# Kernel tuning notes

Measured on AMD Instinct MI355X. Metric: run time of the kernel, lower is better.

Reference implementation:

```python
import jax, jax.numpy as jnp
import numpy as np

N = 50000      # nodes
E = 800000     # edges per view (before self loops)
F_IN = 256     # node feature dim
H = 4          # attention heads
C = 128        # hidden dim (per-head out_channels; concat=False -> mean over heads)
V = 3          # views
NEG_SLOPE = 0.2


def gat_view(x, edge_index, W, a_src, a_dst, b):
    """PyG-style GATConv(heads=H, concat=False) + ELU. Adds self loops."""
    n = x.shape[0]
    loops = jnp.arange(n, dtype=edge_index.dtype)
    src = jnp.concatenate([edge_index[0], loops])  # [E+N]
    dst = jnp.concatenate([edge_index[1], loops])
    h = (x @ W).reshape(n, H, C)                    # [N,H,C]
    s_src = jnp.sum(h * a_src, axis=-1)             # [N,H]
    s_dst = jnp.sum(h * a_dst, axis=-1)             # [N,H]
    e = jax.nn.leaky_relu(s_src[src] + s_dst[dst], NEG_SLOPE)  # [E+N,H]
    # segment softmax over incoming edges of each destination node
    m = jax.ops.segment_max(e, dst, num_segments=n)
    m = jnp.where(jnp.isfinite(m), m, 0.0)
    ex = jnp.exp(e - m[dst])
    denom = jax.ops.segment_sum(ex, dst, num_segments=n)
    alpha = ex / jnp.maximum(denom[dst], 1e-16)     # [E+N,H]
    out = jax.ops.segment_sum(h[src] * alpha[:, :, None], dst, num_segments=n)  # [N,H,C]
    return jax.nn.elu(out.mean(axis=1) + b)         # [N,C]


def setup_inputs() -> dict:
    key = jax.random.key(0)
    ks = jax.random.split(key, 12)
    d = {
        "x": jax.random.normal(ks[0], (N, F_IN), dtype=jnp.float32),
        "edge_index0": jax.random.randint(ks[1], (2, E), 0, N, dtype=jnp.int32),
        "edge_index1": jax.random.randint(ks[2], (2, E), 0, N, dtype=jnp.int32),
        "edge_index2": jax.random.randint(ks[3], (2, E), 0, N, dtype=jnp.int32),
        "W": jax.random.normal(ks[4], (V, F_IN, H * C), dtype=jnp.float32) * 0.05,
        "a_src": jax.random.normal(ks[5], (V, H, C), dtype=jnp.float32) * 0.05,
        "a_dst": jax.random.normal(ks[6], (V, H, C), dtype=jnp.float32) * 0.05,
        "b": jnp.zeros((V, C), dtype=jnp.float32),
        "fus_w": jax.random.normal(ks[7], (C, 1), dtype=jnp.float32) * 0.05,
        "fus_b": jnp.zeros((1,), dtype=jnp.float32),
        "cls_w1": jax.random.normal(ks[8], (C, C // 2), dtype=jnp.float32) * 0.05,
        "cls_b1": jnp.zeros((C // 2,), dtype=jnp.float32),
        "cls_w2": jax.random.normal(ks[9], (C // 2, 2), dtype=jnp.float32) * 0.05,
        "cls_b2": jnp.zeros((2,), dtype=jnp.float32),
    }
    return d


def reference(x, edge_index0, edge_index1, edge_index2, W, a_src, a_dst, b,
              fus_w, fus_b, cls_w1, cls_b1, cls_w2, cls_b2):
    eis = [edge_index0, edge_index1, edge_index2]
    views = [gat_view(x, eis[v], W[v], a_src[v], a_dst[v], b[v]) for v in range(V)]
    stacked = jnp.stack(views, axis=1)                     # [N,V,C]
    scores = jnp.squeeze(stacked @ fus_w, -1) + fus_b      # [N,V]
    weights = jax.nn.softmax(scores, axis=1)               # view attention
    fused = jnp.sum(stacked * weights[..., None], axis=1)  # [N,C]
    hcls = jax.nn.relu(fused @ cls_w1 + cls_b1)            # dropout = identity (eval)
    logits = hcls @ cls_w2 + cls_b2                        # [N,2]
    return logits, weights
```

## Files before the change

kernel.cpp:

```cpp
#include <hip/hip_runtime.h>
#include <math.h>

#define NN 50000
#define EE 800000
#define FIN 256
#define HH 4
#define CC 128
#define HC 512
#define VV 3

#define NB 196
#define SPB 256
#define CAP 4608
#define EPB 8192

typedef __attribute__((ext_vector_type(8))) short short8;
typedef __attribute__((ext_vector_type(4))) float f32x4;
typedef __attribute__((ext_vector_type(2))) float f32x2;

__device__ __forceinline__ float lrelu(float x){ return x > 0.f ? x : 0.2f*x; }

__device__ __forceinline__ unsigned short f2bf(float f){
  unsigned u = __float_as_uint(f);
  u += 0x7fffu + ((u >> 16) & 1);
  return (unsigned short)(u >> 16);
}
__device__ __forceinline__ float bf2f(short b){
  return __uint_as_float(((unsigned)b & 0xffffu) << 16);
}

__device__ __forceinline__ float wave_sum64(float v){
#pragma unroll
  for (int off = 32; off; off >>= 1) v += __shfl_xor(v, off);
  return v;
}

__device__ __forceinline__ void async16(void* lds, const void* g){
  __builtin_amdgcn_global_load_lds(
      (const __attribute__((address_space(1))) unsigned*)g,
      (__attribute__((address_space(3))) unsigned*)lds, 16, 0, 0);
}

__global__ __launch_bounds__(256) void cast_x(const float* __restrict__ x,
                                              unsigned short* __restrict__ xb){
  int t = blockIdx.x * 256 + threadIdx.x;
  float4 v = *(const float4*)&x[(size_t)t * 4];
  ushort4 o;
  o.x = f2bf(v.x); o.y = f2bf(v.y); o.z = f2bf(v.z); o.w = f2bf(v.w);
  *(ushort4*)&xb[(size_t)t * 4] = o;
}

__global__ __launch_bounds__(256) void prep_w_all(const float* __restrict__ W,
                                                  unsigned short* __restrict__ wp){
  int t = blockIdx.x * 256 + threadIdx.x;
  int v = t >> 17;
  int tl = t & 131071;
  int k = tl >> 9, n = tl & 511;
  wp[(size_t)v * (FIN * HC) + (size_t)(k >> 5) * (HC * 32) + n * 32 + (k & 31)] = f2bf(W[t]);
}

__global__ __launch_bounds__(256) void gemm_mfma_scores(
    const unsigned short* __restrict__ xb, const unsigned short* __restrict__ wp_all,
    unsigned char* __restrict__ hb_all,
    const float* __restrict__ a_src, const float* __restrict__ a_dst,
    float* __restrict__ ssrc_all, float* __restrict__ sdst_all){
  __shared__ short As[128 * 32];
  __shared__ short Bs[128 * 32];
  __shared__ float sred[2][128][2];
  int tid = threadIdx.x;
  int wave = tid >> 6, lane = tid & 63;
  int l16 = lane & 15, q = lane >> 4;
  int wr = wave >> 1, wc = wave & 1;
  int head = blockIdx.y, v = blockIdx.z;
  int rowBase = blockIdx.x * 128, colBase = head * 128;

  const unsigned short* wp = wp_all + (size_t)v * FIN * HC;
  unsigned char* hb = hb_all + (size_t)v * NN * HC;
  const float* a_src_v = a_src + v * HH * CC;
  const float* a_dst_v = a_dst + v * HH * CC;
  float* ssrc = ssrc_all + (size_t)v * NN * HH;
  float* sdst = sdst_all + (size_t)v * NN * HH;

  int off0 = wave * 2048 + lane * 16;
  int off1 = off0 + 1024;
  int arow0 = off0 >> 6, akb0 = (off0 & 63) >> 1;
  int arow1 = off1 >> 6, akb1 = (off1 & 63) >> 1;
  size_t ga0 = (size_t)min(rowBase + arow0, NN - 1) * FIN + akb0;
  size_t ga1 = (size_t)min(rowBase + arow1, NN - 1) * FIN + akb1;
  const unsigned short* wpc = wp + (size_t)colBase * 32;

  f32x4 acc[4][4] = {};
  for (int kt = 0; kt < 8; kt++){
    async16((char*)As + wave * 2048,        xb + ga0 + kt * 32);
    async16((char*)As + wave * 2048 + 1024, xb + ga1 + kt * 32);
    async16((char*)Bs + wave * 2048,        wpc + (size_t)kt * (HC * 32) + (off0 >> 1));
    async16((char*)Bs + wave * 2048 + 1024, wpc + (size_t)kt * (HC * 32) + (off1 >> 1));
    __syncthreads();
    short8 af[4], bf[4];
#pragma unroll
    for (int i = 0; i < 4; i++)
      af[i] = *(const short8*)&As[(wr * 64 + i * 16 + l16) * 32 + q * 8];
#pragma unroll
    for (int j = 0; j < 4; j++)
      bf[j] = *(const short8*)&Bs[(wc * 64 + j * 16 + l16) * 32 + q * 8];
#pragma unroll
    for (int i = 0; i < 4; i++)
#pragma unroll
      for (int j = 0; j < 4; j++)
        acc[i][j] = __builtin_amdgcn_mfma_f32_16x16x32_bf16(af[i], bf[j], acc[i][j], 0, 0, 0);
    __syncthreads();
  }
#pragma unroll
  for (int i = 0; i < 4; i++){
#pragma unroll
    for (int r = 0; r < 4; r++){
      int row = rowBase + wr * 64 + i * 16 + q * 4 + r;
      if (row < NN){
        int p01 = __builtin_amdgcn_cvt_pk_fp8_f32(acc[i][0][r], acc[i][1][r], 0, false);
        int p23 = __builtin_amdgcn_cvt_pk_fp8_f32(acc[i][2][r], acc[i][3][r], 0, false);
        size_t rb = (size_t)row * HC + colBase + wc * 64 + l16;
        hb[rb +  0] = (unsigned char)(p01 & 0xff);
        hb[rb + 16] = (unsigned char)((p01 >> 8) & 0xff);
        hb[rb + 32] = (unsigned char)(p23 & 0xff);
        hb[rb + 48] = (unsigned char)((p23 >> 8) & 0xff);
      }
    }
  }
  float asv[4], adv[4];
#pragma unroll
  for (int j = 0; j < 4; j++){
    int c = wc * 64 + j * 16 + l16;
    asv[j] = a_src_v[head * CC + c];
    adv[j] = a_dst_v[head * CC + c];
  }
  float ps[4][4], pd[4][4];
#pragma unroll
  for (int i = 0; i < 4; i++)
#pragma unroll
    for (int r = 0; r < 4; r++){
      float s = 0.f, d = 0.f;
#pragma unroll
      for (int j = 0; j < 4; j++){
        s = fmaf(acc[i][j][r], asv[j], s);
        d = fmaf(acc[i][j][r], adv[j], d);
      }
      ps[i][r] = s; pd[i][r] = d;
    }
#pragma unroll
  for (int off = 1; off < 16; off <<= 1)
#pragma unroll
    for (int i = 0; i < 4; i++)
#pragma unroll
      for (int r = 0; r < 4; r++){
        ps[i][r] += __shfl_xor(ps[i][r], off);
        pd[i][r] += __shfl_xor(pd[i][r], off);
      }
  if (l16 == 0){
#pragma unroll
    for (int i = 0; i < 4; i++)
#pragma unroll
      for (int r = 0; r < 4; r++){
        int rl = wr * 64 + i * 16 + q * 4 + r;
        sred[wc][rl][0] = ps[i][r];
        sred[wc][rl][1] = pd[i][r];
      }
  }
  __syncthreads();
  if (tid < 128){
    int row = rowBase + tid;
    if (row < NN){
      ssrc[row * HH + head] = sred[0][tid][0] + sred[1][tid][0];
      sdst[row * HH + head] = sred[0][tid][1] + sred[1][tid][1];
    }
  }
}

__global__ __launch_bounds__(256) void bucket_scatter(const int* __restrict__ e0,
    const int* __restrict__ e1, const int* __restrict__ e2,
    int* __restrict__ gcur, unsigned* __restrict__ pairs){
  int v = blockIdx.y;
  const int* ei = (v == 0) ? e0 : ((v == 1) ? e1 : e2);
  __shared__ int cnt[NB];
  __shared__ int base[NB];
  int tid = threadIdx.x;
  for (int i = tid; i < NB; i += 256) cnt[i] = 0;
  __syncthreads();
  int estart = blockIdx.x * EPB;
  int eend = min(estart + EPB, EE);
  for (int e = estart + tid; e < eend; e += 256)
    atomicAdd(&cnt[ei[EE + e] >> 8], 1);
  __syncthreads();
  for (int i = tid; i < NB; i += 256){
    int c = cnt[i];
    base[i] = (c > 0) ? atomicAdd(&gcur[v * NB + i], c) : 0;
    cnt[i] = 0;
  }
  __syncthreads();
  for (int e = estart + tid; e < eend; e += 256){
    int s = ei[e], d = ei[EE + e];
    int b = d >> 8;
    int off = base[b] + atomicAdd(&cnt[b], 1);
    if (off < CAP)
      pairs[(size_t)(v * NB + b) * CAP + off] = ((unsigned)(d & 255) << 16) | (unsigned)s;
  }
}

__global__ __launch_bounds__(256) void bucket_scan(const int* __restrict__ gcur,
                                                   int* __restrict__ bbase){
  int v = blockIdx.x;
  __shared__ int wsum[4];
  int tid = threadIdx.x, lane = tid & 63, wv = tid >> 6;
  int val = 0;
  if (tid < NB) val = min(gcur[v * NB + tid], CAP) + min(SPB, NN - tid * SPB);
  int x = val;
#pragma unroll
  for (int off = 1; off < 64; off <<= 1){
    int t = __shfl_up(x, off);
    if (lane >= off) x += t;
  }
  if (lane == 63) wsum[wv] = x;
  __syncthreads();
  int pre = 0;
#pragma unroll
  for (int w = 0; w < 4; w++) if (w < wv) pre += wsum[w];
  if (tid < NB) bbase[v * NB + tid] = pre + x - val;
}

__global__ __launch_bounds__(256) void bucket_csr(const int* __restrict__ gcur,
    const int* __restrict__ bbase, const unsigned* __restrict__ pairs,
    int* __restrict__ rowptr_all, int* __restrict__ colx_all){
  int v = blockIdx.y, b = blockIdx.x;
  int* rowptr = rowptr_all + v * (NN + 1);
  int* colx = colx_all + (size_t)v * (EE + NN);
  __shared__ int hist[SPB];
  __shared__ int wsum[4];
  __shared__ int lcol[CAP + SPB];
  int tid = threadIdx.x, lane = tid & 63, wv = tid >> 6;
  int node0 = b << 8;
  int nvalid = min(SPB, NN - node0);
  int cnt = min(gcur[v * NB + b], CAP);
  int base = bbase[v * NB + b];
  const unsigned* pp = pairs + (size_t)(v * NB + b) * CAP;
  hist[tid] = (tid < nvalid) ? 1 : 0;
  __syncthreads();
  for (int i = tid; i < cnt; i += 256)
    atomicAdd(&hist[pp[i] >> 16], 1);
  __syncthreads();
  int val = hist[tid];
  int x = val;
#pragma unroll
  for (int off = 1; off < 64; off <<= 1){
    int t = __shfl_up(x, off);
    if (lane >= off) x += t;
  }
  if (lane == 63) wsum[wv] = x;
  __syncthreads();
  int pre = 0;
#pragma unroll
  for (int w = 0; w < 4; w++) if (w < wv) pre += wsum[w];
  int excl = pre + x - val;
  __syncthreads();
  hist[tid] = excl + ((tid < nvalid) ? 1 : 0);
  if (tid < nvalid){
    rowptr[node0 + tid] = base + excl;
    lcol[excl] = node0 + tid;
  }
  __syncthreads();
  for (int i = tid; i < cnt; i += 256){
    unsigned p = pp[i];
    int pos = atomicAdd(&hist[p >> 16], 1);
    lcol[pos] = (int)(p & 0xffffu);
  }
  __syncthreads();
  int total = cnt + nvalid;
  for (int i = tid; i < total; i += 256) colx[base + i] = lcol[i];
  if (b == NB - 1 && tid == 0) rowptr[NN] = base + total;
}

__global__ __launch_bounds__(256) void aggregate(const unsigned char* __restrict__ hb_all,
    const float* __restrict__ ssrc_all, const float* __restrict__ sdst_all,
    const int* __restrict__ rowptr_all, const int* __restrict__ colx_all,
    const float* __restrict__ bb, unsigned short* __restrict__ vout_all){
  int v = blockIdx.y;
  const unsigned char* hb = hb_all + (size_t)v * NN * HC;
  const float* ssrc = ssrc_all + (size_t)v * NN * HH;
  const float* sdst = sdst_all + (size_t)v * NN * HH;
  const int* rowptr = rowptr_all + v * (NN + 1);
  const int* colx = colx_all + (size_t)v * (EE + NN);
  const float* bv = bb + v * CC;
  unsigned short* voutv = vout_all + (size_t)v * NN * CC;

  int wave = threadIdx.x >> 6, lane = threadIdx.x & 63;
  int node = blockIdx.x * 4 + wave;
  int start = rowptr[node];
  int deg = rowptr[node + 1] - start;
  int myh = lane >> 4;
  float sdh = sdst[node * HH + myh];
  float acc[8] = {0.f, 0.f, 0.f, 0.f, 0.f, 0.f, 0.f, 0.f};
  float dsum = 0.f;

#define AGG_FMA(CH, CE) { \
    f32x2 p0 = __builtin_amdgcn_cvt_pk_f32_fp8(CH.x, false); \
    f32x2 p1 = __builtin_amdgcn_cvt_pk_f32_fp8(CH.x, true); \
    f32x2 p2 = __builtin_amdgcn_cvt_pk_f32_fp8(CH.y, false); \
    f32x2 p3 = __builtin_amdgcn_cvt_pk_f32_fp8(CH.y, true); \
    acc[0] = fmaf(CE, p0[0], acc[0]); \
    acc[1] = fmaf(CE, p0[1], acc[1]); \
    acc[2] = fmaf(CE, p1[0], acc[2]); \
    acc[3] = fmaf(CE, p1[1], acc[3]); \
    acc[4] = fmaf(CE, p2[0], acc[4]); \
    acc[5] = fmaf(CE, p2[1], acc[5]); \
    acc[6] = fmaf(CE, p3[0], acc[6]); \
    acc[7] = fmaf(CE, p3[1], acc[7]); }

  if (deg <= 64){
    int cpre = (lane < deg) ? colx[start + lane] : 0;
    uint2 h0, h1, h2, h3, h4, h5, h6, h7;
    float s0, s1, s2, s3, s4, s5, s6, s7;
#define AGG_PRO(HP, SP, P) { \
    int sp = __shfl(cpre, min(P, deg - 1)); \
    HP = *(const uint2*)&hb[(size_t)(unsigned)(sp * HC) + lane * 8]; \
    SP = ssrc[sp * HH + myh]; }
    AGG_PRO(h0, s0, 0) AGG_PRO(h1, s1, 1) AGG_PRO(h2, s2, 2) AGG_PRO(h3, s3, 3)
    AGG_PRO(h4, s4, 4) AGG_PRO(h5, s5, 5) AGG_PRO(h6, s6, 6) AGG_PRO(h7, s7, 7)
#undef AGG_PRO
#define AGG_STEP(HP, SP, P) { \
    float ce = __expf(lrelu(SP + sdh)); \
    dsum += ce; \
    uint2 ch = HP; \
    int ni = i + 8 + P; \
    if (ni < deg){ \
      int ns = __shfl(cpre, ni); \
      HP = *(const uint2*)&hb[(size_t)(unsigned)(ns * HC) + lane * 8]; \
      SP = ssrc[ns * HH + myh]; \
    } \
    AGG_FMA(ch, ce) }
    int i = 0;
    for (; i + 8 <= deg; i += 8){
      AGG_STEP(h0, s0, 0) AGG_STEP(h1, s1, 1) AGG_STEP(h2, s2, 2) AGG_STEP(h3, s3, 3)
      AGG_STEP(h4, s4, 4) AGG_STEP(h5, s5, 5) AGG_STEP(h6, s6, 6) AGG_STEP(h7, s7, 7)
    }
#undef AGG_STEP
    int rem = deg - i;
#define AGG_TAIL(HP, SP, P) if (rem > P){ \
    float ce = __expf(lrelu(SP + sdh)); \
    dsum += ce; \
    AGG_FMA(HP, ce) }
    AGG_TAIL(h0, s0, 0) AGG_TAIL(h1, s1, 1) AGG_TAIL(h2, s2, 2) AGG_TAIL(h3, s3, 3)
    AGG_TAIL(h4, s4, 4) AGG_TAIL(h5, s5, 5) AGG_TAIL(h6, s6, 6)
#undef AGG_TAIL
  } else {
    for (int i = 0; i < deg; i++){
      int src = colx[start + i];
      float sv = ssrc[src * HH + myh];
      float ce = __expf(lrelu(sv + sdh));
      dsum += ce;
      uint2 ch = *(const uint2*)&hb[(size_t)(unsigned)(src * HC) + lane * 8];
      AGG_FMA(ch, ce)
    }
  }
#undef AGG_FMA
  float rinv = 0.25f / fmaxf(dsum, 1e-16f);
#pragma unroll
  for (int j = 0; j < 8; j++) acc[j] *= rinv;
#pragma unroll
  for (int off = 16; off < 64; off <<= 1){
#pragma unroll
    for (int j = 0; j < 8; j++) acc[j] += __shfl_xor(acc[j], off);
  }
  if (lane < 16){
    int c0 = lane * 8;
    short8 o;
#pragma unroll
    for (int j = 0; j < 8; j++){
      float vv = acc[j] + bv[c0 + j];
      float e = vv > 0.f ? vv : (__expf(vv) - 1.f);
      o[j] = (short)f2bf(e);
    }
    *(short8*)&voutv[(size_t)node * CC + c0] = o;
  }
}

__global__ __launch_bounds__(256) void fuse_classify(const unsigned short* __restrict__ vb,
    const float* __restrict__ fw, const float* __restrict__ fb,
    const float* __restrict__ w1, const float* __restrict__ b1,
    const float* __restrict__ w2, const float* __restrict__ b2,
    float* __restrict__ out){
  __shared__ float sw1[CC * 64];
  __shared__ float sfused[4][CC];
  int tid = threadIdx.x;
  for (int i = tid * 4; i < CC * 64; i += 1024)
    *(float4*)&sw1[i] = *(const float4*)&w1[i];
  __syncthreads();
  int wave = tid >> 6, lane = tid & 63;
  int node = blockIdx.x * 4 + wave;
  unsigned r0 = *(const unsigned*)&vb[(size_t)(0 * NN + node) * CC + lane * 2];
  unsigned r1 = *(const unsigned*)&vb[(size_t)(1 * NN + node) * CC + lane * 2];
  unsigned r2 = *(const unsigned*)&vb[(size_t)(2 * NN + node) * CC + lane * 2];
  float v0x = bf2f((short)(r0 & 0xffffu)), v0y = bf2f((short)(r0 >> 16));
  float v1x = bf2f((short)(r1 & 0xffffu)), v1y = bf2f((short)(r1 >> 16));
  float v2x = bf2f((short)(r2 & 0xffffu)), v2y = bf2f((short)(r2 >> 16));
  float fwa = fw[lane * 2], fwb = fw[lane * 2 + 1];
  float s0 = wave_sum64(v0x * fwa + v0y * fwb) + fb[0];
  float s1 = wave_sum64(v1x * fwa + v1y * fwb) + fb[0];
  float s2 = wave_sum64(v2x * fwa + v2y * fwb) + fb[0];
  float mx = fmaxf(s0, fmaxf(s1, s2));
  float e0 = __expf(s0 - mx), e1 = __expf(s1 - mx), e2 = __expf(s2 - mx);
  float rs = 1.f / (e0 + e1 + e2);
  float w0 = e0 * rs, w1v = e1 * rs, w2v = e2 * rs;
  float f0 = w0 * v0x + w1v * v1x + w2v * v2x;
  float f1 = w0 * v0y + w1v * v1y + w2v * v2y;
  sfused[wave][lane * 2]     = f0;
  sfused[wave][lane * 2 + 1] = f1;
  if (lane < 3){
    float wv = (lane == 0) ? w0 : ((lane == 1) ? w1v : w2v);
    out[2 * NN + node * 3 + lane] = wv;
  }
  __syncthreads();
  float hc = b1[lane];
#pragma unroll 8
  for (int c = 0; c < CC; c++)
    hc = fmaf(sfused[wave][c], sw1[c * 64 + lane], hc);
  hc = fmaxf(hc, 0.f);
  float l0 = wave_sum64(hc * w2[lane * 2]);
  float l1 = wave_sum64(hc * w2[lane * 2 + 1]);
  if (lane == 0){
    out[node * 2]     = l0 + b2[0];
    out[node * 2 + 1] = l1 + b2[1];
  }
}

extern "C" void kernel_launch(void* const* d_in, const int* in_sizes, int n_in,
                              void* d_out, int out_size, void* d_ws, size_t ws_size,
                              hipStream_t stream){
  const float* x      = (const float*)d_in[0];
  const int*   e0     = (const int*)d_in[1];
  const int*   e1     = (const int*)d_in[2];
  const int*   e2     = (const int*)d_in[3];
  const float* W      = (const float*)d_in[4];
  const float* a_src  = (const float*)d_in[5];
  const float* a_dst  = (const float*)d_in[6];
  const float* bb     = (const float*)d_in[7];
  const float* fus_w  = (const float*)d_in[8];
  const float* fus_b  = (const float*)d_in[9];
  const float* cls_w1 = (const float*)d_in[10];
  const float* cls_b1 = (const float*)d_in[11];
  const float* cls_w2 = (const float*)d_in[12];
  const float* cls_b2 = (const float*)d_in[13];
  float* out = (float*)d_out;

  unsigned short* xb = (unsigned short*)d_ws;
  unsigned char* hb  = (unsigned char*)(xb + (size_t)NN * FIN);
  unsigned short* wp = (unsigned short*)(hb + (size_t)VV * NN * HC);
  float* ssrc = (float*)(wp + (size_t)VV * FIN * HC);
  float* sdst = ssrc + (size_t)VV * NN * HH;
  int* gcur   = (int*)(sdst + (size_t)VV * NN * HH);
  int* bbase  = gcur + VV * NB;
  int* rowptr = bbase + VV * NB;
  int* colx   = rowptr + VV * (NN + 1);
  unsigned* pairs = (unsigned*)(colx + (size_t)VV * (EE + NN));
  unsigned short* voutb = (unsigned short*)pairs;

  hipMemsetAsync(gcur, 0, (size_t)VV * NB * sizeof(int), stream);
  cast_x<<<12500, 256, 0, stream>>>(x, xb);
  prep_w_all<<<1536, 256, 0, stream>>>(W, wp);
  dim3 p1grid((EE + EPB - 1) / EPB, 3);
  bucket_scatter<<<p1grid, 256, 0, stream>>>(e0, e1, e2, gcur, pairs);
  bucket_scan<<<3, 256, 0, stream>>>(gcur, bbase);
  dim3 p2grid(NB, 3);
  bucket_csr<<<p2grid, 256, 0, stream>>>(gcur, bbase, pairs, rowptr, colx);

  dim3 ggrid(391, 4, 3);
  gemm_mfma_scores<<<ggrid, 256, 0, stream>>>(xb, wp, hb, a_src, a_dst, ssrc, sdst);
  dim3 agrid(12500, 3);
  aggregate<<<agrid, 256, 0, stream>>>(hb, ssrc, sdst, rowptr, colx, bb, voutb);
  fuse_classify<<<12500, 256, 0, stream>>>(voutb, fus_w, fus_b, cls_w1, cls_b1,
                                           cls_w2, cls_b2, out);
}
```

Before: 545.4 us.

## Load GEMM fragments directly with register double-buffering, pre-scale CSR indices, batch fuse_classify nodes

The GEMM drops its LDS staging and barriers and instead loads MFMA fragments straight from global memory into registers, double-buffered across k-steps. CSR column indices are stored pre-multiplied by 4, so the aggregate kernel computes addresses with shifts, and its separate high-degree path is folded into one prefetching loop that reads colx once the degree exceeds 64. The aggregate FMAs use packed f32x2 operations. fuse_classify processes 8 node groups per block so the W1 copy into LDS is amortised, and the bucket scatter uses a smaller EPB. Risks: no A/B reuse through LDS means more global traffic in the GEMM, and the __syncthreads before reading sfused is replaced by a waitcnt, which relies on each wave reading only its own row.

```diff
diff --git a/kernel.cpp b/kernel.cpp
--- a/kernel.cpp
+++ b/kernel.cpp
@@ -12,13 +12,11 @@
 #define NB 196
 #define SPB 256
 #define CAP 4608
-#define EPB 8192
+#define EPB 2048
 
 typedef __attribute__((ext_vector_type(8))) short short8;
 typedef __attribute__((ext_vector_type(4))) float f32x4;
 typedef __attribute__((ext_vector_type(2))) float f32x2;
-
-__device__ __forceinline__ float lrelu(float x){ return x > 0.f ? x : 0.2f*x; }
 
 __device__ __forceinline__ unsigned short f2bf(float f){
   unsigned u = __float_as_uint(f);
@@ -33,12 +31,6 @@
 #pragma unroll
   for (int off = 32; off; off >>= 1) v += __shfl_xor(v, off);
   return v;
-}
-
-__device__ __forceinline__ void async16(void* lds, const void* g){
-  __builtin_amdgcn_global_load_lds(
-      (const __attribute__((address_space(1))) unsigned*)g,
-      (__attribute__((address_space(3))) unsigned*)lds, 16, 0, 0);
 }
 
 __global__ __launch_bounds__(256) void cast_x(const float* __restrict__ x,
@@ -64,8 +56,6 @@
     unsigned char* __restrict__ hb_all,
     const float* __restrict__ a_src, const float* __restrict__ a_dst,
     float* __restrict__ ssrc_all, float* __restrict__ sdst_all){
-  __shared__ short As[128 * 32];
-  __shared__ short Bs[128 * 32];
   __shared__ float sred[2][128][2];
   int tid = threadIdx.x;
   int wave = tid >> 6, lane = tid & 63;
@@ -81,34 +71,40 @@
   float* ssrc = ssrc_all + (size_t)v * NN * HH;
   float* sdst = sdst_all + (size_t)v * NN * HH;
 
-  int off0 = wave * 2048 + lane * 16;
-  int off1 = off0 + 1024;
-  int arow0 = off0 >> 6, akb0 = (off0 & 63) >> 1;
-  int arow1 = off1 >> 6, akb1 = (off1 & 63) >> 1;
-  size_t ga0 = (size_t)min(rowBase + arow0, NN - 1) * FIN + akb0;
-  size_t ga1 = (size_t)min(rowBase + arow1, NN - 1) * FIN + akb1;
-  const unsigned short* wpc = wp + (size_t)colBase * 32;
-
+  const unsigned short* ap[4];
+  const unsigned short* bp[4];
+#pragma unroll
+  for (int i = 0; i < 4; i++){
+    int row = min(rowBase + wr * 64 + i * 16 + l16, NN - 1);
+    ap[i] = xb + (size_t)row * FIN + q * 8;
+  }
+#pragma unroll
+  for (int j = 0; j < 4; j++){
+    int col = colBase + wc * 64 + j * 16 + l16;
+    bp[j] = wp + (size_t)col * 32 + q * 8;
+  }
+  short8 af[2][4], bf[2][4];
+#pragma unroll
+  for (int i = 0; i < 4; i++){
+    af[0][i] = *(const short8*)(ap[i]);
+    bf[0][i] = *(const short8*)(bp[i]);
+  }
   f32x4 acc[4][4] = {};
+#pragma unroll
   for (int kt = 0; kt < 8; kt++){
-    async16((char*)As + wave * 2048,        xb + ga0 + kt * 32);
-    async16((char*)As + wave * 2048 + 1024, xb + ga1 + kt * 32);
-    async16((char*)Bs + wave * 2048,        wpc + (size_t)kt * (HC * 32) + (off0 >> 1));
-    async16((char*)Bs + wave * 2048 + 1024, wpc + (size_t)kt * (HC * 32) + (off1 >> 1));
-    __syncthreads();
-    short8 af[4], bf[4];
+    int cur = kt & 1, nxt = cur ^ 1;
+    if (kt < 7){
+#pragma unroll
+      for (int i = 0; i < 4; i++){
+        af[nxt][i] = *(const short8*)(ap[i] + (kt + 1) * 32);
+        bf[nxt][i] = *(const short8*)(bp[i] + (size_t)(kt + 1) * (HC * 32));
+      }
+    }
 #pragma unroll
     for (int i = 0; i < 4; i++)
-      af[i] = *(const short8*)&As[(wr * 64 + i * 16 + l16) * 32 + q * 8];
-#pragma unroll
-    for (int j = 0; j < 4; j++)
-      bf[j] = *(const short8*)&Bs[(wc * 64 + j * 16 + l16) * 32 + q * 8];
-#pragma unroll
-    for (int i = 0; i < 4; i++)
 #pragma unroll
       for (int j = 0; j < 4; j++)
-        acc[i][j] = __builtin_amdgcn_mfma_f32_16x16x32_bf16(af[i], bf[j], acc[i][j], 0, 0, 0);
-    __syncthreads();
+        acc[i][j] = __builtin_amdgcn_mfma_f32_16x16x32_bf16(af[cur][i], bf[cur][j], acc[i][j], 0, 0, 0);
   }
 #pragma unroll
   for (int i = 0; i < 4; i++){
@@ -263,13 +259,13 @@
   hist[tid] = excl + ((tid < nvalid) ? 1 : 0);
   if (tid < nvalid){
     rowptr[node0 + tid] = base + excl;
-    lcol[excl] = node0 + tid;
+    lcol[excl] = (node0 + tid) << 2;
   }
   __syncthreads();
   for (int i = tid; i < cnt; i += 256){
     unsigned p = pp[i];
     int pos = atomicAdd(&hist[p >> 16], 1);
-    lcol[pos] = (int)(p & 0xffffu);
+    lcol[pos] = (int)(p & 0xffffu) << 2;
   }
   __syncthreads();
   int total = cnt + nvalid;
@@ -287,93 +283,82 @@
   const float* sdst = sdst_all + (size_t)v * NN * HH;
   const int* rowptr = rowptr_all + v * (NN + 1);
   const int* colx = colx_all + (size_t)v * (EE + NN);
-  const float* bv = bb + v * CC;
-  unsigned short* voutv = vout_all + (size_t)v * NN * CC;
 
   int wave = threadIdx.x >> 6, lane = threadIdx.x & 63;
   int node = blockIdx.x * 4 + wave;
   int start = rowptr[node];
   int deg = rowptr[node + 1] - start;
   int myh = lane >> 4;
+  int l8 = lane * 8;
   float sdh = sdst[node * HH + myh];
-  float acc[8] = {0.f, 0.f, 0.f, 0.f, 0.f, 0.f, 0.f, 0.f};
+  f32x2 acc2[4] = {};
   float dsum = 0.f;
-
-#define AGG_FMA(CH, CE) { \
-    f32x2 p0 = __builtin_amdgcn_cvt_pk_f32_fp8(CH.x, false); \
-    f32x2 p1 = __builtin_amdgcn_cvt_pk_f32_fp8(CH.x, true); \
-    f32x2 p2 = __builtin_amdgcn_cvt_pk_f32_fp8(CH.y, false); \
-    f32x2 p3 = __builtin_amdgcn_cvt_pk_f32_fp8(CH.y, true); \
-    acc[0] = fmaf(CE, p0[0], acc[0]); \
-    acc[1] = fmaf(CE, p0[1], acc[1]); \
-    acc[2] = fmaf(CE, p1[0], acc[2]); \
-    acc[3] = fmaf(CE, p1[1], acc[3]); \
-    acc[4] = fmaf(CE, p2[0], acc[4]); \
-    acc[5] = fmaf(CE, p2[1], acc[5]); \
-    acc[6] = fmaf(CE, p3[0], acc[6]); \
-    acc[7] = fmaf(CE, p3[1], acc[7]); }
-
-  if (deg <= 64){
-    int cpre = (lane < deg) ? colx[start + lane] : 0;
-    uint2 h0, h1, h2, h3, h4, h5, h6, h7;
-    float s0, s1, s2, s3, s4, s5, s6, s7;
+  int cpre = (lane < deg) ? colx[start + lane] : 0;
+  uint2 h0, h1, h2, h3, h4, h5, h6, h7;
+  float s0, s1, s2, s3, s4, s5, s6, s7;
 #define AGG_PRO(HP, SP, P) { \
-    int sp = __shfl(cpre, min(P, deg - 1)); \
-    HP = *(const uint2*)&hb[(size_t)(unsigned)(sp * HC) + lane * 8]; \
-    SP = ssrc[sp * HH + myh]; }
-    AGG_PRO(h0, s0, 0) AGG_PRO(h1, s1, 1) AGG_PRO(h2, s2, 2) AGG_PRO(h3, s3, 3)
-    AGG_PRO(h4, s4, 4) AGG_PRO(h5, s5, 5) AGG_PRO(h6, s6, 6) AGG_PRO(h7, s7, 7)
+    int sp4 = __shfl(cpre, min(P, deg - 1)); \
+    HP = *(const uint2*)&hb[((size_t)(unsigned)sp4 << 7) + l8]; \
+    SP = ssrc[sp4 + myh]; }
+  AGG_PRO(h0, s0, 0) AGG_PRO(h1, s1, 1) AGG_PRO(h2, s2, 2) AGG_PRO(h3, s3, 3)
+  AGG_PRO(h4, s4, 4) AGG_PRO(h5, s5, 5) AGG_PRO(h6, s6, 6) AGG_PRO(h7, s7, 7)
 #undef AGG_PRO
+#define AGG_FMA(CH, E2) { \
+    acc2[0] = __builtin_elementwise_fma(E2, __builtin_amdgcn_cvt_pk_f32_fp8(CH.x, false), acc2[0]); \
+    acc2[1] = __builtin_elementwise_fma(E2, __builtin_amdgcn_cvt_pk_f32_fp8(CH.x, true),  acc2[1]); \
+    acc2[2] = __builtin_elementwise_fma(E2, __builtin_amdgcn_cvt_pk_f32_fp8(CH.y, false), acc2[2]); \
+    acc2[3] = __builtin_elementwise_fma(E2, __builtin_amdgcn_cvt_pk_f32_fp8(CH.y, true),  acc2[3]); }
 #define AGG_STEP(HP, SP, P) { \
-    float ce = __expf(lrelu(SP + sdh)); \
+    float xx = SP + sdh; \
+    float ce = __expf(fmaxf(xx, 0.2f * xx)); \
     dsum += ce; \
     uint2 ch = HP; \
     int ni = i + 8 + P; \
     if (ni < deg){ \
-      int ns = __shfl(cpre, ni); \
-      HP = *(const uint2*)&hb[(size_t)(unsigned)(ns * HC) + lane * 8]; \
-      SP = ssrc[ns * HH + myh]; \
+      int sp4; \
+      if (ni < 64) sp4 = __shfl(cpre, ni); else sp4 = colx[start + ni]; \
+      HP = *(const uint2*)&hb[((size_t)(unsigned)sp4 << 7) + l8]; \
+      SP = ssrc[sp4 + myh]; \
     } \
-    AGG_FMA(ch, ce) }
-    int i = 0;
-    for (; i + 8 <= deg; i += 8){
-      AGG_STEP(h0, s0, 0) AGG_STEP(h1, s1, 1) AGG_STEP(h2, s2, 2) AGG_STEP(h3, s3, 3)
-      AGG_STEP(h4, s4, 4) AGG_STEP(h5, s5, 5) AGG_STEP(h6, s6, 6) AGG_STEP(h7, s7, 7)
-    }
+    f32x2 e2 = {ce, ce}; \
+    AGG_FMA(ch, e2) }
+#define AGG_TAIL(HP, SP, P) if (rem > P){ \
+    float xx = SP + sdh; \
+    float ce = __expf(fmaxf(xx, 0.2f * xx)); \
+    dsum += ce; \
+    f32x2 e2 = {ce, ce}; \
+    AGG_FMA(HP, e2) }
+  int i = 0;
+  for (; i + 8 <= deg; i += 8){
+    AGG_STEP(h0, s0, 0) AGG_STEP(h1, s1, 1) AGG_STEP(h2, s2, 2) AGG_STEP(h3, s3, 3)
+    AGG_STEP(h4, s4, 4) AGG_STEP(h5, s5, 5) AGG_STEP(h6, s6, 6) AGG_STEP(h7, s7, 7)
+  }
+  int rem = deg - i;
+  AGG_TAIL(h0, s0, 0) AGG_TAIL(h1, s1, 1) AGG_TAIL(h2, s2, 2) AGG_TAIL(h3, s3, 3)
+  AGG_TAIL(h4, s4, 4) AGG_TAIL(h5, s5, 5) AGG_TAIL(h6, s6, 6)
 #undef AGG_STEP
-    int rem = deg - i;
-#define AGG_TAIL(HP, SP, P) if (rem > P){ \
-    float ce = __expf(lrelu(SP + sdh)); \
-    dsum += ce; \
-    AGG_FMA(HP, ce) }
-    AGG_TAIL(h0, s0, 0) AGG_TAIL(h1, s1, 1) AGG_TAIL(h2, s2, 2) AGG_TAIL(h3, s3, 3)
-    AGG_TAIL(h4, s4, 4) AGG_TAIL(h5, s5, 5) AGG_TAIL(h6, s6, 6)
 #undef AGG_TAIL
-  } else {
-    for (int i = 0; i < deg; i++){
-      int src = colx[start + i];
-      float sv = ssrc[src * HH + myh];
-      float ce = __expf(lrelu(sv + sdh));
-      dsum += ce;
-      uint2 ch = *(const uint2*)&hb[(size_t)(unsigned)(src * HC) + lane * 8];
-      AGG_FMA(ch, ce)
-    }
-  }
 #undef AGG_FMA
   float rinv = 0.25f / fmaxf(dsum, 1e-16f);
-#pragma unroll
-  for (int j = 0; j < 8; j++) acc[j] *= rinv;
+  float accs[8];
+#pragma unroll
+  for (int j = 0; j < 4; j++){
+    accs[2 * j]     = acc2[j][0] * rinv;
+    accs[2 * j + 1] = acc2[j][1] * rinv;
+  }
 #pragma unroll
   for (int off = 16; off < 64; off <<= 1){
 #pragma unroll
-    for (int j = 0; j < 8; j++) acc[j] += __shfl_xor(acc[j], off);
+    for (int j = 0; j < 8; j++) accs[j] += __shfl_xor(accs[j], off);
   }
   if (lane < 16){
+    const float* bv = bb + v * CC;
+    unsigned short* voutv = vout_all + (size_t)v * NN * CC;
     int c0 = lane * 8;
     short8 o;
 #pragma unroll
     for (int j = 0; j < 8; j++){
-      float vv = acc[j] + bv[c0 + j];
+      float vv = accs[j] + bv[c0 + j];
       float e = vv > 0.f ? vv : (__expf(vv) - 1.f);
       o[j] = (short)f2bf(e);
     }
@@ -393,40 +378,46 @@
     *(float4*)&sw1[i] = *(const float4*)&w1[i];
   __syncthreads();
   int wave = tid >> 6, lane = tid & 63;
-  int node = blockIdx.x * 4 + wave;
-  unsigned r0 = *(const unsigned*)&vb[(size_t)(0 * NN + node) * CC + lane * 2];
-  unsigned r1 = *(const unsigned*)&vb[(size_t)(1 * NN + node) * CC + lane * 2];
-  unsigned r2 = *(const unsigned*)&vb[(size_t)(2 * NN + node) * CC + lane * 2];
-  float v0x = bf2f((short)(r0 & 0xffffu)), v0y = bf2f((short)(r0 >> 16));
-  float v1x = bf2f((short)(r1 & 0xffffu)), v1y = bf2f((short)(r1 >> 16));
-  float v2x = bf2f((short)(r2 & 0xffffu)), v2y = bf2f((short)(r2 >> 16));
   float fwa = fw[lane * 2], fwb = fw[lane * 2 + 1];
-  float s0 = wave_sum64(v0x * fwa + v0y * fwb) + fb[0];
-  float s1 = wave_sum64(v1x * fwa + v1y * fwb) + fb[0];
-  float s2 = wave_sum64(v2x * fwa + v2y * fwb) + fb[0];
-  float mx = fmaxf(s0, fmaxf(s1, s2));
-  float e0 = __expf(s0 - mx), e1 = __expf(s1 - mx), e2 = __expf(s2 - mx);
-  float rs = 1.f / (e0 + e1 + e2);
-  float w0 = e0 * rs, w1v = e1 * rs, w2v = e2 * rs;
-  float f0 = w0 * v0x + w1v * v1x + w2v * v2x;
-  float f1 = w0 * v0y + w1v * v1y + w2v * v2y;
-  sfused[wave][lane * 2]     = f0;
-  sfused[wave][lane * 2 + 1] = f1;
-  if (lane < 3){
-    float wv = (lane == 0) ? w0 : ((lane == 1) ? w1v : w2v);
-    out[2 * NN + node * 3 + lane] = wv;
-  }
-  __syncthreads();
-  float hc = b1[lane];
+  float w2a = w2[lane * 2], w2b = w2[lane * 2 + 1];
+  float b1l = b1[lane];
+  for (int g = 0; g < 8; g++){
+    int node = blockIdx.x * 32 + g * 4 + wave;
+    if (node < NN){
+      unsigned r0 = *(const unsigned*)&vb[(size_t)(0 * NN + node) * CC + lane * 2];
+      unsigned r1 = *(const unsigned*)&vb[(size_t)(1 * NN + node) * CC + lane * 2];
+      unsigned r2 = *(const unsigned*)&vb[(size_t)(2 * NN + node) * CC + lane * 2];
+      float v0x = bf2f((short)(r0 & 0xffffu)), v0y = bf2f((short)(r0 >> 16));
+      float v1x = bf2f((short)(r1 & 0xffffu)), v1y = bf2f((short)(r1 >> 16));
+      float v2x = bf2f((short)(r2 & 0xffffu)), v2y = bf2f((short)(r2 >> 16));
+      float s0 = wave_sum64(v0x * fwa + v0y * fwb) + fb[0];
+      float s1 = wave_sum64(v1x * fwa + v1y * fwb) + fb[0];
+      float s2 = wave_sum64(v2x * fwa + v2y * fwb) + fb[0];
+      float mx = fmaxf(s0, fmaxf(s1, s2));
+      float e0 = __expf(s0 - mx), e1 = __expf(s1 - mx), e2 = __expf(s2 - mx);
+      float rs = 1.f / (e0 + e1 + e2);
+      float w0 = e0 * rs, w1v = e1 * rs, w2v = e2 * rs;
+      float f0 = w0 * v0x + w1v * v1x + w2v * v2x;
+      float f1 = w0 * v0y + w1v * v1y + w2v * v2y;
+      sfused[wave][lane * 2]     = f0;
+      sfused[wave][lane * 2 + 1] = f1;
+      if (lane < 3){
+        float wv = (lane == 0) ? w0 : ((lane == 1) ? w1v : w2v);
+        out[2 * NN + node * 3 + lane] = wv;
+      }
+      __builtin_amdgcn_s_waitcnt(0);
+      float hc = b1l;
 #pragma unroll 8
-  for (int c = 0; c < CC; c++)
-    hc = fmaf(sfused[wave][c], sw1[c * 64 + lane], hc);
-  hc = fmaxf(hc, 0.f);
-  float l0 = wave_sum64(hc * w2[lane * 2]);
-  float l1 = wave_sum64(hc * w2[lane * 2 + 1]);
-  if (lane == 0){
-    out[node * 2]     = l0 + b2[0];
-    out[node * 2 + 1] = l1 + b2[1];
+      for (int c = 0; c < CC; c++)
+        hc = fmaf(sfused[wave][c], sw1[c * 64 + lane], hc);
+      hc = fmaxf(hc, 0.f);
+      float l0 = wave_sum64(hc * w2a);
+      float l1 = wave_sum64(hc * w2b);
+      if (lane == 0){
+        out[node * 2]     = l0 + b2[0];
+        out[node * 2 + 1] = l1 + b2[1];
+      }
+    }
   }
 }
 
@@ -474,6 +465,6 @@
   gemm_mfma_scores<<<ggrid, 256, 0, stream>>>(xb, wp, hb, a_src, a_dst, ssrc, sdst);
   dim3 agrid(12500, 3);
   aggregate<<<agrid, 256, 0, stream>>>(hb, ssrc, sdst, rowptr, colx, bb, voutb);
-  fuse_classify<<<12500, 256, 0, stream>>>(voutb, fus_w, fus_b, cls_w1, cls_b1,
-                                           cls_w2, cls_b2, out);
-}
+  fuse_classify<<<1563, 256, 0, stream>>>(voutb, fus_w, fus_b, cls_w1, cls_b1,
+                                          cls_w2, cls_b2, out);
+}
```

Result: slower. 677.7 us (+24.3%).

## Load GEMM fragments directly from global, amortize classifier weights, shrink scatter chunk

Applied to the files above, without the earlier changes.

The GEMM drops its LDS staging and barriers and loads MFMA fragments straight from global memory into registers, with the k-loop fully unrolled. fuse_classify now handles 32 nodes per block, so the 32 KB W1 copy into LDS is paid once per 32 nodes instead of once per 4. The edge-scatter chunk size shrinks so the scatter kernel gets more blocks. Risks: the GEMM loses LDS sharing and issues redundant, less coalesced global loads. The classifier now relies on a waitcnt rather than a barrier to order its per-wave LDS writes and reads.

```diff
diff --git a/kernel.cpp b/kernel.cpp
--- a/kernel.cpp
+++ b/kernel.cpp
@@ -12,7 +12,7 @@
 #define NB 196
 #define SPB 256
 #define CAP 4608
-#define EPB 8192
+#define EPB 2048
 
 typedef __attribute__((ext_vector_type(8))) short short8;
 typedef __attribute__((ext_vector_type(4))) float f32x4;
@@ -33,12 +33,6 @@
 #pragma unroll
   for (int off = 32; off; off >>= 1) v += __shfl_xor(v, off);
   return v;
-}
-
-__device__ __forceinline__ void async16(void* lds, const void* g){
-  __builtin_amdgcn_global_load_lds(
-      (const __attribute__((address_space(1))) unsigned*)g,
-      (__attribute__((address_space(3))) unsigned*)lds, 16, 0, 0);
 }
 
 __global__ __launch_bounds__(256) void cast_x(const float* __restrict__ x,
@@ -64,8 +58,6 @@
     unsigned char* __restrict__ hb_all,
     const float* __restrict__ a_src, const float* __restrict__ a_dst,
     float* __restrict__ ssrc_all, float* __restrict__ sdst_all){
-  __shared__ short As[128 * 32];
-  __shared__ short Bs[128 * 32];
   __shared__ float sred[2][128][2];
   int tid = threadIdx.x;
   int wave = tid >> 6, lane = tid & 63;
@@ -81,34 +73,32 @@
   float* ssrc = ssrc_all + (size_t)v * NN * HH;
   float* sdst = sdst_all + (size_t)v * NN * HH;
 
-  int off0 = wave * 2048 + lane * 16;
-  int off1 = off0 + 1024;
-  int arow0 = off0 >> 6, akb0 = (off0 & 63) >> 1;
-  int arow1 = off1 >> 6, akb1 = (off1 & 63) >> 1;
-  size_t ga0 = (size_t)min(rowBase + arow0, NN - 1) * FIN + akb0;
-  size_t ga1 = (size_t)min(rowBase + arow1, NN - 1) * FIN + akb1;
-  const unsigned short* wpc = wp + (size_t)colBase * 32;
-
+  const unsigned short* ap[4];
+  const unsigned short* bp[4];
+#pragma unroll
+  for (int i = 0; i < 4; i++){
+    int row = min(rowBase + wr * 64 + i * 16 + l16, NN - 1);
+    ap[i] = xb + (size_t)row * FIN + q * 8;
+  }
+#pragma unroll
+  for (int j = 0; j < 4; j++){
+    int col = colBase + wc * 64 + j * 16 + l16;
+    bp[j] = wp + (size_t)col * 32 + q * 8;
+  }
   f32x4 acc[4][4] = {};
+#pragma unroll
   for (int kt = 0; kt < 8; kt++){
-    async16((char*)As + wave * 2048,        xb + ga0 + kt * 32);
-    async16((char*)As + wave * 2048 + 1024, xb + ga1 + kt * 32);
-    async16((char*)Bs + wave * 2048,        wpc + (size_t)kt * (HC * 32) + (off0 >> 1));
-    async16((char*)Bs + wave * 2048 + 1024, wpc + (size_t)kt * (HC * 32) + (off1 >> 1));
-    __syncthreads();
     short8 af[4], bf[4];
 #pragma unroll
-    for (int i = 0; i < 4; i++)
-      af[i] = *(const short8*)&As[(wr * 64 + i * 16 + l16) * 32 + q * 8];
-#pragma unroll
-    for (int j = 0; j < 4; j++)
-      bf[j] = *(const short8*)&Bs[(wc * 64 + j * 16 + l16) * 32 + q * 8];
+    for (int i = 0; i < 4; i++){
+      af[i] = *(const short8*)(ap[i] + kt * 32);
+      bf[i] = *(const short8*)(bp[i] + (size_t)kt * (HC * 32));
+    }
 #pragma unroll
     for (int i = 0; i < 4; i++)
 #pragma unroll
       for (int j = 0; j < 4; j++)
         acc[i][j] = __builtin_amdgcn_mfma_f32_16x16x32_bf16(af[i], bf[j], acc[i][j], 0, 0, 0);
-    __syncthreads();
   }
 #pragma unroll
   for (int i = 0; i < 4; i++){
@@ -287,8 +277,6 @@
   const float* sdst = sdst_all + (size_t)v * NN * HH;
   const int* rowptr = rowptr_all + v * (NN + 1);
   const int* colx = colx_all + (size_t)v * (EE + NN);
-  const float* bv = bb + v * CC;
-  unsigned short* voutv = vout_all + (size_t)v * NN * CC;
 
   int wave = threadIdx.x >> 6, lane = threadIdx.x & 63;
   int node = blockIdx.x * 4 + wave;
@@ -369,6 +357,8 @@
     for (int j = 0; j < 8; j++) acc[j] += __shfl_xor(acc[j], off);
   }
   if (lane < 16){
+    const float* bv = bb + v * CC;
+    unsigned short* voutv = vout_all + (size_t)v * NN * CC;
     int c0 = lane * 8;
     short8 o;
 #pragma unroll
@@ -393,40 +383,46 @@
     *(float4*)&sw1[i] = *(const float4*)&w1[i];
   __syncthreads();
   int wave = tid >> 6, lane = tid & 63;
-  int node = blockIdx.x * 4 + wave;
-  unsigned r0 = *(const unsigned*)&vb[(size_t)(0 * NN + node) * CC + lane * 2];
-  unsigned r1 = *(const unsigned*)&vb[(size_t)(1 * NN + node) * CC + lane * 2];
-  unsigned r2 = *(const unsigned*)&vb[(size_t)(2 * NN + node) * CC + lane * 2];
-  float v0x = bf2f((short)(r0 & 0xffffu)), v0y = bf2f((short)(r0 >> 16));
-  float v1x = bf2f((short)(r1 & 0xffffu)), v1y = bf2f((short)(r1 >> 16));
-  float v2x = bf2f((short)(r2 & 0xffffu)), v2y = bf2f((short)(r2 >> 16));
   float fwa = fw[lane * 2], fwb = fw[lane * 2 + 1];
-  float s0 = wave_sum64(v0x * fwa + v0y * fwb) + fb[0];
-  float s1 = wave_sum64(v1x * fwa + v1y * fwb) + fb[0];
-  float s2 = wave_sum64(v2x * fwa + v2y * fwb) + fb[0];
-  float mx = fmaxf(s0, fmaxf(s1, s2));
-  float e0 = __expf(s0 - mx), e1 = __expf(s1 - mx), e2 = __expf(s2 - mx);
-  float rs = 1.f / (e0 + e1 + e2);
-  float w0 = e0 * rs, w1v = e1 * rs, w2v = e2 * rs;
-  float f0 = w0 * v0x + w1v * v1x + w2v * v2x;
-  float f1 = w0 * v0y + w1v * v1y + w2v * v2y;
-  sfused[wave][lane * 2]     = f0;
-  sfused[wave][lane * 2 + 1] = f1;
-  if (lane < 3){
-    float wv = (lane == 0) ? w0 : ((lane == 1) ? w1v : w2v);
-    out[2 * NN + node * 3 + lane] = wv;
-  }
-  __syncthreads();
-  float hc = b1[lane];
+  float w2a = w2[lane * 2], w2b = w2[lane * 2 + 1];
+  float b1l = b1[lane];
+  for (int g = 0; g < 8; g++){
+    int node = blockIdx.x * 32 + g * 4 + wave;
+    if (node < NN){
+      unsigned r0 = *(const unsigned*)&vb[(size_t)(0 * NN + node) * CC + lane * 2];
+      unsigned r1 = *(const unsigned*)&vb[(size_t)(1 * NN + node) * CC + lane * 2];
+      unsigned r2 = *(const unsigned*)&vb[(size_t)(2 * NN + node) * CC + lane * 2];
+      float v0x = bf2f((short)(r0 & 0xffffu)), v0y = bf2f((short)(r0 >> 16));
+      float v1x = bf2f((short)(r1 & 0xffffu)), v1y = bf2f((short)(r1 >> 16));
+      float v2x = bf2f((short)(r2 & 0xffffu)), v2y = bf2f((short)(r2 >> 16));
+      float s0 = wave_sum64(v0x * fwa + v0y * fwb) + fb[0];
+      float s1 = wave_sum64(v1x * fwa + v1y * fwb) + fb[0];
+      float s2 = wave_sum64(v2x * fwa + v2y * fwb) + fb[0];
+      float mx = fmaxf(s0, fmaxf(s1, s2));
+      float e0 = __expf(s0 - mx), e1 = __expf(s1 - mx), e2 = __expf(s2 - mx);
+      float rs = 1.f / (e0 + e1 + e2);
+      float w0 = e0 * rs, w1v = e1 * rs, w2v = e2 * rs;
+      float f0 = w0 * v0x + w1v * v1x + w2v * v2x;
+      float f1 = w0 * v0y + w1v * v1y + w2v * v2y;
+      sfused[wave][lane * 2]     = f0;
+      sfused[wave][lane * 2 + 1] = f1;
+      if (lane < 3){
+        float wv = (lane == 0) ? w0 : ((lane == 1) ? w1v : w2v);
+        out[2 * NN + node * 3 + lane] = wv;
+      }
+      __builtin_amdgcn_s_waitcnt(0);
+      float hc = b1l;
 #pragma unroll 8
-  for (int c = 0; c < CC; c++)
-    hc = fmaf(sfused[wave][c], sw1[c * 64 + lane], hc);
-  hc = fmaxf(hc, 0.f);
-  float l0 = wave_sum64(hc * w2[lane * 2]);
-  float l1 = wave_sum64(hc * w2[lane * 2 + 1]);
-  if (lane == 0){
-    out[node * 2]     = l0 + b2[0];
-    out[node * 2 + 1] = l1 + b2[1];
+      for (int c = 0; c < CC; c++)
+        hc = fmaf(sfused[wave][c], sw1[c * 64 + lane], hc);
+      hc = fmaxf(hc, 0.f);
+      float l0 = wave_sum64(hc * w2a);
+      float l1 = wave_sum64(hc * w2b);
+      if (lane == 0){
+        out[node * 2]     = l0 + b2[0];
+        out[node * 2 + 1] = l1 + b2[1];
+      }
+    }
   }
 }
 
@@ -474,6 +470,6 @@
   gemm_mfma_scores<<<ggrid, 256, 0, stream>>>(xb, wp, hb, a_src, a_dst, ssrc, sdst);
   dim3 agrid(12500, 3);
   aggregate<<<agrid, 256, 0, stream>>>(hb, ssrc, sdst, rowptr, colx, bb, voutb);
-  fuse_classify<<<12500, 256, 0, stream>>>(voutb, fus_w, fus_b, cls_w1, cls_b1,
-                                           cls_w2, cls_b2, out);
-}
+  fuse_classify<<<1563, 256, 0, stream>>>(voutb, fus_w, fus_b, cls_w1, cls_b1,
+                                          cls_w2, cls_b2, out);
+}
```

After: 582.4 us. 6.8% more time.
